# Performance work log

Hardware: AMD Instinct MI355X
Metric: run time of the kernel (lower is better)

## Reference

```python
import jax, jax.numpy as jnp
import numpy as np
from jax import lax

HIDDEN = 1024
STATE = 64
BATCH = 16
SEQ = 2048
DT_MIN, DT_MAX = 0.001, 0.1


def setup_inputs() -> dict:
    key = jax.random.key(0)
    k = jax.random.split(key, 6)
    x = jax.random.normal(k[0], (BATCH, SEQ, HIDDEN), dtype=jnp.float32)
    A = jax.random.normal(k[1], (STATE, STATE), dtype=jnp.float32) * 0.01
    B = jax.random.normal(k[2], (STATE, HIDDEN), dtype=jnp.float32) * 0.01
    C = jax.random.normal(k[3], (HIDDEN, STATE), dtype=jnp.float32) * 0.01
    D = jnp.ones((HIDDEN,), dtype=jnp.float32)
    log_dt = jax.random.uniform(k[4], (HIDDEN,), dtype=jnp.float32) * (
        np.log(DT_MAX) - np.log(DT_MIN)
    ) + np.log(DT_MIN)
    return {"x": x, "A": A, "B": B, "C": C, "D": D, "log_dt": log_dt}


def reference(x, A, B, C, D, log_dt):
    # x: (B, T, H)
    dt = jnp.exp(log_dt)                                  # (H,)
    A_bar = jax.scipy.linalg.expm(A * dt.mean())          # (N, N)
    B_bar = B * dt[None, :]                               # (N, H)
    # Precompute input injection for all timesteps: (B, T, N)
    u = jnp.einsum("bth,nh->btn", x, B_bar)

    def step(state, u_t):
        # state: (B, N); u_t: (B, N)
        state = state @ A_bar.T + u_t
        return state, state

    init = jnp.zeros((x.shape[0], A.shape[0]), dtype=x.dtype)
    _, states = lax.scan(step, init, jnp.swapaxes(u, 0, 1))  # (T, B, N)
    states = jnp.swapaxes(states, 0, 1)                      # (B, T, N)
    return jnp.einsum("btn,hn->bth", states, C) + D * x
```

## Files before the change

kernel.cpp:

```cpp
#include <hip/hip_runtime.h>


#define H   1024
#define NS  64
#define NB  16
#define TT  2048
#define LCH 64
#define KCH 32

typedef __attribute__((ext_vector_type(8))) short bf16x8;
typedef __attribute__((ext_vector_type(4))) float f32x4;
typedef __attribute__((ext_vector_type(2))) unsigned int u32x2;

#define WS_ABAR 0
#define WS_AL   4096
#define WS_F    8192
#define WS_P    40960
#define WS_U    73728
#define WS_S    2170880

__device__ __forceinline__ unsigned short f2bf(float x) {
  union { float f; unsigned u; } v; v.f = x;
  unsigned r = (v.u + 0x7FFFu + ((v.u >> 16) & 1u)) >> 16;
  return (unsigned short)r;
}

__device__ __forceinline__ bf16x8 packbf8(f32x4 a, f32x4 b) {
  bf16x8 r;
  r[0] = (short)f2bf(a[0]); r[1] = (short)f2bf(a[1]);
  r[2] = (short)f2bf(a[2]); r[3] = (short)f2bf(a[3]);
  r[4] = (short)f2bf(b[0]); r[5] = (short)f2bf(b[1]);
  r[6] = (short)f2bf(b[2]); r[7] = (short)f2bf(b[3]);
  return r;
}

__device__ __forceinline__ u32x2 packbf4(f32x4 v) {
  u32x2 r;
  r[0] = (unsigned)f2bf(v[0]) | ((unsigned)f2bf(v[1]) << 16);
  r[1] = (unsigned)f2bf(v[2]) | ((unsigned)f2bf(v[3]) << 16);
  return r;
}

__device__ __forceinline__ f32x4 mfma16(bf16x8 a, bf16x8 b, f32x4 c) {
  return __builtin_amdgcn_mfma_f32_16x16x32_bf16(a, b, c, 0, 0, 0);
}

__device__ void prep_block(const float* Ain, const float* ldt, float* ws, int which) {
  __shared__ float Mb[64 * 68];
  __shared__ short Tl[64 * 72];
  const int lane = threadIdx.x;
  const int cq = lane >> 4, cl = lane & 15;

  float s = 0.f;
  for (int j = 0; j < 16; ++j) s += expf(ldt[lane + j * 64]);
  for (int off = 32; off; off >>= 1) s += __shfl_down(s, off);
  float dtm = __shfl(s, 0) * (1.0f / 1024.0f);
  float scale = which ? dtm * (float)LCH : dtm;

  for (int idx = lane; idx < 4096; idx += 64) {
    int r = idx >> 6, c = idx & 63;
    float v = Ain[idx] * scale;
    Mb[c * 68 + r] = v;
    Tl[r * 72 + c] = (short)f2bf(v);
  }

  float E[16][4];
  for (int mt = 0; mt < 4; ++mt)
    for (int nt = 0; nt < 4; ++nt)
      for (int r = 0; r < 4; ++r) {
        int row = mt * 16 + cq * 4 + r, col = nt * 16 + cl;
        E[mt * 4 + nt][r] = (row == col ? 1.f : 0.f) + Ain[row * 64 + col] * scale;
      }

  __asm volatile("s_waitcnt lgkmcnt(0)" ::: "memory");

  for (int it = 2; it <= 12; ++it) {
    bf16x8 af[4][2];
    for (int mt = 0; mt < 4; ++mt)
      for (int kh = 0; kh < 2; ++kh)
        af[mt][kh] = *(const bf16x8*)&Tl[(mt * 16 + cl) * 72 + kh * 32 + cq * 8];
    float inv = 1.0f / (float)it;
    bf16x8 bfr[4][2];
    for (int nt = 0; nt < 4; ++nt)
      for (int kh = 0; kh < 2; ++kh) {
        const float* p = &Mb[(nt * 16 + cl) * 68 + kh * 32 + cq * 8];
        f32x4 a = *(const f32x4*)p;
        f32x4 b = *(const f32x4*)(p + 4);
        bfr[nt][kh] = packbf8(a * inv, b * inv);
      }
    f32x4 zero = {0.f, 0.f, 0.f, 0.f};
    f32x4 acc[16];
    for (int i = 0; i < 16; ++i) acc[i] = zero;
    for (int mt = 0; mt < 4; ++mt)
      for (int nt = 0; nt < 4; ++nt) {
        acc[mt * 4 + nt] = mfma16(af[mt][0], bfr[nt][0], acc[mt * 4 + nt]);
        acc[mt * 4 + nt] = mfma16(af[mt][1], bfr[nt][1], acc[mt * 4 + nt]);
      }
    __asm volatile("s_waitcnt lgkmcnt(0)" ::: "memory");
    for (int mt = 0; mt < 4; ++mt)
      for (int nt = 0; nt < 4; ++nt)
        for (int r = 0; r < 4; ++r) {
          float t = acc[mt * 4 + nt][r];
          E[mt * 4 + nt][r] += t;
          Tl[(mt * 16 + cq * 4 + r) * 72 + nt * 16 + cl] = (short)f2bf(t);
        }
    __asm volatile("s_waitcnt lgkmcnt(0)" ::: "memory");
  }

  float* dst = ws + (which ? WS_AL : WS_ABAR);
  for (int mt = 0; mt < 4; ++mt)
    for (int nt = 0; nt < 4; ++nt)
      for (int r = 0; r < 4; ++r)
        dst[(mt * 16 + cq * 4 + r) * 64 + nt * 16 + cl] = E[mt * 4 + nt][r];
}

__device__ void gemm_u(const float* x, const float* Bm, const float* ldt, float* u2, int bid) {
  __shared__ short xl[64 * 40];
  __shared__ short bl[64 * 40];
  const int tid = threadIdx.x;
  const int bt0 = bid * 64;
  const int wid = tid >> 6, lane = tid & 63;
  const int cq = lane >> 4, cl = lane & 15;
  const int mst = tid >> 2, k0 = (tid & 3) * 8;

  f32x4 zero = {0.f, 0.f, 0.f, 0.f};
  f32x4 acc[4];
  for (int i = 0; i < 4; ++i) acc[i] = zero;

  const float* xrow = x + (long)(bt0 + mst) * H + k0;
  const float* brow = Bm + (long)mst * H + k0;

  for (int hc = 0; hc < 32; ++hc) {
    int h0 = hc * 32;
    f32x4 xa = *(const f32x4*)(xrow + h0);
    f32x4 xb = *(const f32x4*)(xrow + h0 + 4);
    f32x4 ba = *(const f32x4*)(brow + h0);
    f32x4 bb = *(const f32x4*)(brow + h0 + 4);
    f32x4 da, db;
    for (int j = 0; j < 4; ++j) {
      da[j] = expf(ldt[h0 + k0 + j]);
      db[j] = expf(ldt[h0 + k0 + 4 + j]);
    }
    *(bf16x8*)&xl[mst * 40 + k0] = packbf8(xa, xb);
    *(bf16x8*)&bl[mst * 40 + k0] = packbf8(ba * da, bb * db);
    __syncthreads();
    bf16x8 afr = *(const bf16x8*)&xl[(wid * 16 + cl) * 40 + cq * 8];
    for (int nt = 0; nt < 4; ++nt) {
      bf16x8 bfr = *(const bf16x8*)&bl[(nt * 16 + cl) * 40 + cq * 8];
      acc[nt] = mfma16(afr, bfr, acc[nt]);
    }
    __syncthreads();
  }
  for (int nt = 0; nt < 4; ++nt)
    for (int r = 0; r < 4; ++r) {
      int bt = bt0 + wid * 16 + cq * 4 + r;
      int t = bt & (TT - 1), b = bt >> 11;
      u2[(long)(t * 16 + b) * 64 + nt * 16 + cl] = acc[nt][r];
    }
}

__global__ __launch_bounds__(256) void k1(const float* x, const float* Ain, const float* Bm,
                                          const float* ldt, float* ws) {
  if (blockIdx.x < 2) {
    if (threadIdx.x < 64) prep_block(Ain, ldt, ws, blockIdx.x);
    return;
  }
  gemm_u(x, Bm, ldt, ws + WS_U, blockIdx.x - 2);
}

__device__ __forceinline__ void load_RF(const float* Amat, bf16x8 Rf[4][2], int cq, int cl) {
  for (int mt = 0; mt < 4; ++mt)
    for (int kh = 0; kh < 2; ++kh) {
      int m = mt * 16 + cl;
      int kb = kh * 32 + cq * 8;
      f32x4 v0 = *(const f32x4*)&Amat[m * 64 + kb];
      f32x4 v1 = *(const f32x4*)&Amat[m * 64 + kb + 4];
      for (int j = 0; j < 4; ++j) {
        if (m == kb + j) v0[j] -= 1.f;
        if (m == kb + 4 + j) v1[j] -= 1.f;
      }
      Rf[mt][kh] = packbf8(v0, v1);
    }
}

__device__ __forceinline__ void scan_step(f32x4 Z[4], const bf16x8 Rf[4][2], short* Zl,
                                          const f32x4 U[4], int cq, int cl) {
  for (int t = 0; t < 4; ++t)
    *(u32x2*)&Zl[cl * 72 + t * 16 + cq * 4] = packbf4(Z[t]);
  __asm volatile("s_waitcnt lgkmcnt(0)" ::: "memory");
  bf16x8 zf0 = *(const bf16x8*)&Zl[cl * 72 + cq * 8];
  bf16x8 zf1 = *(const bf16x8*)&Zl[cl * 72 + 32 + cq * 8];
  for (int t = 0; t < 4; ++t) Z[t] += U[t];
  for (int mt = 0; mt < 4; ++mt) {
    Z[mt] = mfma16(Rf[mt][0], zf0, Z[mt]);
    Z[mt] = mfma16(Rf[mt][1], zf1, Z[mt]);
  }
}

__global__ __launch_bounds__(64) void scan_local_k(float* ws) {
  const float* Abar = ws + WS_ABAR;
  const float* u2 = ws + WS_U;
  float* F = ws + WS_F;
  __shared__ short Zl[16 * 72];
  const int lane = threadIdx.x, cq = lane >> 4, cl = lane & 15;
  const int c = blockIdx.x;
  bf16x8 Rf[4][2];
  load_RF(Abar, Rf, cq, cl);
  f32x4 zero = {0.f, 0.f, 0.f, 0.f};
  f32x4 Z[4], U[4], Un[4];
  for (int t = 0; t < 4; ++t) Z[t] = zero;
  const float* ub = u2 + (long)c * LCH * 1024 + cl * 64 + cq * 4;
  for (int t = 0; t < 4; ++t) U[t] = *(const f32x4*)(ub + t * 16);
  for (int ti = 0; ti < LCH; ++ti) {
    const float* un = ub + (ti + 1) * 1024;
    for (int t = 0; t < 4; ++t) Un[t] = *(const f32x4*)(un + t * 16);
    scan_step(Z, Rf, Zl, U, cq, cl);
    for (int t = 0; t < 4; ++t) U[t] = Un[t];
  }
  for (int t = 0; t < 4; ++t)
    *(f32x4*)&F[(long)c * 1024 + cl * 64 + t * 16 + cq * 4] = Z[t];
}

__global__ __launch_bounds__(64) void scan_chunks_k(float* ws) {
  const float* AL = ws + WS_AL;
  const float* F = ws + WS_F;
  float* P = ws + WS_P;
  __shared__ short Zl[16 * 72];
  const int lane = threadIdx.x, cq = lane >> 4, cl = lane & 15;
  bf16x8 Rf[4][2];
  load_RF(AL, Rf, cq, cl);
  f32x4 zero = {0.f, 0.f, 0.f, 0.f};
  f32x4 Z[4], U[4];
  for (int t = 0; t < 4; ++t) Z[t] = zero;
  for (int c = 0; c < KCH; ++c) {
    long off = (long)c * 1024 + cl * 64 + cq * 4;
    for (int t = 0; t < 4; ++t) *(f32x4*)&P[off + t * 16] = Z[t];
    for (int t = 0; t < 4; ++t) U[t] = *(const f32x4*)&F[off + t * 16];
    scan_step(Z, Rf, Zl, U, cq, cl);
  }
}

__global__ __launch_bounds__(64) void scan_final_k(float* ws) {
  const float* Abar = ws + WS_ABAR;
  const float* u2 = ws + WS_U;
  const float* P = ws + WS_P;
  float* S2 = ws + WS_S;
  __shared__ short Zl[16 * 72];
  const int lane = threadIdx.x, cq = lane >> 4, cl = lane & 15;
  const int c = blockIdx.x;
  bf16x8 Rf[4][2];
  load_RF(Abar, Rf, cq, cl);
  f32x4 Z[4], U[4], Un[4];
  long poff = (long)c * 1024 + cl * 64 + cq * 4;
  for (int t = 0; t < 4; ++t) Z[t] = *(const f32x4*)&P[poff + t * 16];
  const float* ub = u2 + (long)c * LCH * 1024 + cl * 64 + cq * 4;
  float* sb = S2 + (long)c * LCH * 1024 + cl * 64 + cq * 4;
  for (int t = 0; t < 4; ++t) U[t] = *(const f32x4*)(ub + t * 16);
  for (int ti = 0; ti < LCH; ++ti) {
    const float* un = ub + (ti + 1) * 1024;
    for (int t = 0; t < 4; ++t) Un[t] = *(const f32x4*)(un + t * 16);
    scan_step(Z, Rf, Zl, U, cq, cl);
    float* so = sb + ti * 1024;
    for (int t = 0; t < 4; ++t) *(f32x4*)(so + t * 16) = Z[t];
    for (int t = 0; t < 4; ++t) U[t] = Un[t];
  }
}

__global__ __launch_bounds__(256) void out_proj_k(const float* ws, const float* Cm,
                                                  const float* Dv, const float* x, float* out) {
  const float* S2 = ws + WS_S;
  __shared__ short sl[64 * 72];
  __shared__ short cls[128 * 72];
  const int tid = threadIdx.x;
  const int bid = blockIdx.x;
  const int bt0 = (bid & 511) * 64;
  const int h0 = (bid >> 9) * 128;
  const int wid = tid >> 6, lane = tid & 63;
  const int cq = lane >> 4, cl = lane & 15;

  {
    int m = tid >> 2, k0 = (tid & 3) * 16;
    int bt = bt0 + m, t = bt & (TT - 1), b = bt >> 11;
    const float* sr = S2 + (long)(t * 16 + b) * 64 + k0;
    f32x4 a0 = *(const f32x4*)(sr);
    f32x4 a1 = *(const f32x4*)(sr + 4);
    f32x4 a2 = *(const f32x4*)(sr + 8);
    f32x4 a3 = *(const f32x4*)(sr + 12);
    *(bf16x8*)&sl[m * 72 + k0] = packbf8(a0, a1);
    *(bf16x8*)&sl[m * 72 + k0 + 8] = packbf8(a2, a3);

    int hl = tid >> 1, kc = (tid & 1) * 32;
    const float* cr = Cm + (long)(h0 + hl) * 64 + kc;
    f32x4 c0 = *(const f32x4*)(cr);
    f32x4 c1 = *(const f32x4*)(cr + 4);
    f32x4 c2 = *(const f32x4*)(cr + 8);
    f32x4 c3 = *(const f32x4*)(cr + 12);
    f32x4 c4 = *(const f32x4*)(cr + 16);
    f32x4 c5 = *(const f32x4*)(cr + 20);
    f32x4 c6 = *(const f32x4*)(cr + 24);
    f32x4 c7 = *(const f32x4*)(cr + 28);
    *(bf16x8*)&cls[hl * 72 + kc] = packbf8(c0, c1);
    *(bf16x8*)&cls[hl * 72 + kc + 8] = packbf8(c2, c3);
    *(bf16x8*)&cls[hl * 72 + kc + 16] = packbf8(c4, c5);
    *(bf16x8*)&cls[hl * 72 + kc + 24] = packbf8(c6, c7);
  }
  __syncthreads();

  bf16x8 af0 = *(const bf16x8*)&sl[(wid * 16 + cl) * 72 + cq * 8];
  bf16x8 af1 = *(const bf16x8*)&sl[(wid * 16 + cl) * 72 + 32 + cq * 8];
  f32x4 zero = {0.f, 0.f, 0.f, 0.f};
  for (int nt = 0; nt < 8; ++nt) {
    bf16x8 b0 = *(const bf16x8*)&cls[(nt * 16 + cl) * 72 + cq * 8];
    bf16x8 b1 = *(const bf16x8*)&cls[(nt * 16 + cl) * 72 + 32 + cq * 8];
    f32x4 acc = zero;
    acc = mfma16(af0, b0, acc);
    acc = mfma16(af1, b1, acc);
    int h = h0 + nt * 16 + cl;
    float d = Dv[h];
    for (int r = 0; r < 4; ++r) {
      long bt = bt0 + wid * 16 + cq * 4 + r;
      long idx = bt * H + h;
      out[idx] = acc[r] + d * x[idx];
    }
  }
}

extern "C" void kernel_launch(void* const* d_in, const int* in_sizes, int n_in,
                              void* d_out, int out_size, void* d_ws, size_t ws_size,
                              hipStream_t stream) {
  const float* x = (const float*)d_in[0];
  const float* A = (const float*)d_in[1];
  const float* Bm = (const float*)d_in[2];
  const float* Cm = (const float*)d_in[3];
  const float* Dv = (const float*)d_in[4];
  const float* ldt = (const float*)d_in[5];
  float* out = (float*)d_out;
  float* ws = (float*)d_ws;

  k1<<<dim3(2 + 512), dim3(256), 0, stream>>>(x, A, Bm, ldt, ws);
  scan_local_k<<<dim3(KCH), dim3(64), 0, stream>>>(ws);
  scan_chunks_k<<<dim3(1), dim3(64), 0, stream>>>(ws);
  scan_final_k<<<dim3(KCH), dim3(64), 0, stream>>>(ws);
  out_proj_k<<<dim3(4096), dim3(256), 0, stream>>>(ws, Cm, Dv, x, out);
}
```

Baseline: 533.2 us.

## Pre-convert B and C to bf16, store states in bf16, drop LDS staging

A new prologue kernel computes B scaled by dt and converts B and C to bf16 once, writing them into the workspace. The u projection and the output projection now load MFMA fragments straight from global memory instead of staging through LDS with block barriers. Scan states are written as bf16 rather than fp32, which halves the state traffic between the scan and the output projection. In exchange there is one extra launch, B and C are re-read from cache by every block, and the stored states lose precision.

```diff
diff --git a/kernel.cpp b/kernel.cpp
--- a/kernel.cpp
+++ b/kernel.cpp
@@ -18,6 +18,8 @@
 #define WS_P    40960
 #define WS_U    73728
 #define WS_S    2170880
+#define WS_BBF  8192
+#define WS_CBF  3219456
 
 __device__ __forceinline__ unsigned short f2bf(float x) {
   union { float f; unsigned u; } v; v.f = x;
@@ -43,6 +45,20 @@
 
 __device__ __forceinline__ f32x4 mfma16(bf16x8 a, bf16x8 b, f32x4 c) {
   return __builtin_amdgcn_mfma_f32_16x16x32_bf16(a, b, c, 0, 0, 0);
+}
+
+__global__ __launch_bounds__(256) void k0(const float* Bm, const float* Cm,
+                                          const float* ldt, float* ws) {
+  short* Bbf = (short*)(ws + WS_BBF);
+  short* Cbf = (short*)(ws + WS_CBF);
+  const int idx = (blockIdx.x * 256 + threadIdx.x) * 4;
+  f32x4 b = *(const f32x4*)(Bm + idx);
+  f32x4 l = *(const f32x4*)(ldt + (idx & (H - 1)));
+  f32x4 bb;
+  for (int j = 0; j < 4; ++j) bb[j] = b[j] * expf(l[j]);
+  *(u32x2*)&Bbf[idx] = packbf4(bb);
+  f32x4 c = *(const f32x4*)(Cm + idx);
+  *(u32x2*)&Cbf[idx] = packbf4(c);
 }
 
 __device__ void prep_block(const float* Ain, const float* ldt, float* ws, int which) {
@@ -114,58 +130,47 @@
         dst[(mt * 16 + cq * 4 + r) * 64 + nt * 16 + cl] = E[mt * 4 + nt][r];
 }
 
-__device__ void gemm_u(const float* x, const float* Bm, const float* ldt, float* u2, int bid) {
-  __shared__ short xl[64 * 40];
-  __shared__ short bl[64 * 40];
+__device__ void gemm_u(const float* x, const float* ws, float* u2, int bid) {
+  const short* Bbf = (const short*)(ws + WS_BBF);
   const int tid = threadIdx.x;
-  const int bt0 = bid * 64;
   const int wid = tid >> 6, lane = tid & 63;
   const int cq = lane >> 4, cl = lane & 15;
-  const int mst = tid >> 2, k0 = (tid & 3) * 8;
+  const int bt0 = bid * 64 + wid * 16;
+
+  const float* xr = x + (long)(bt0 + cl) * H + cq * 8;
+  const short* br = Bbf + cq * 8;
 
   f32x4 zero = {0.f, 0.f, 0.f, 0.f};
   f32x4 acc[4];
   for (int i = 0; i < 4; ++i) acc[i] = zero;
 
-  const float* xrow = x + (long)(bt0 + mst) * H + k0;
-  const float* brow = Bm + (long)mst * H + k0;
-
-  for (int hc = 0; hc < 32; ++hc) {
-    int h0 = hc * 32;
-    f32x4 xa = *(const f32x4*)(xrow + h0);
-    f32x4 xb = *(const f32x4*)(xrow + h0 + 4);
-    f32x4 ba = *(const f32x4*)(brow + h0);
-    f32x4 bb = *(const f32x4*)(brow + h0 + 4);
-    f32x4 da, db;
-    for (int j = 0; j < 4; ++j) {
-      da[j] = expf(ldt[h0 + k0 + j]);
-      db[j] = expf(ldt[h0 + k0 + 4 + j]);
+#pragma unroll 4
+  for (int ks = 0; ks < 32; ++ks) {
+    const int k0 = ks * 32;
+    f32x4 xa = *(const f32x4*)(xr + k0);
+    f32x4 xb = *(const f32x4*)(xr + k0 + 4);
+    bf16x8 af = packbf8(xa, xb);
+    for (int nt = 0; nt < 4; ++nt) {
+      bf16x8 bf = *(const bf16x8*)(br + (nt * 16 + cl) * H + k0);
+      acc[nt] = mfma16(af, bf, acc[nt]);
     }
-    *(bf16x8*)&xl[mst * 40 + k0] = packbf8(xa, xb);
-    *(bf16x8*)&bl[mst * 40 + k0] = packbf8(ba * da, bb * db);
-    __syncthreads();
-    bf16x8 afr = *(const bf16x8*)&xl[(wid * 16 + cl) * 40 + cq * 8];
-    for (int nt = 0; nt < 4; ++nt) {
-      bf16x8 bfr = *(const bf16x8*)&bl[(nt * 16 + cl) * 40 + cq * 8];
-      acc[nt] = mfma16(afr, bfr, acc[nt]);
-    }
-    __syncthreads();
-  }
+  }
+
   for (int nt = 0; nt < 4; ++nt)
     for (int r = 0; r < 4; ++r) {
-      int bt = bt0 + wid * 16 + cq * 4 + r;
-      int t = bt & (TT - 1), b = bt >> 11;
+      int obt = bt0 + cq * 4 + r;
+      int t = obt & (TT - 1), b = obt >> 11;
       u2[(long)(t * 16 + b) * 64 + nt * 16 + cl] = acc[nt][r];
     }
 }
 
-__global__ __launch_bounds__(256) void k1(const float* x, const float* Ain, const float* Bm,
+__global__ __launch_bounds__(256) void k1(const float* x, const float* Ain,
                                           const float* ldt, float* ws) {
   if (blockIdx.x < 2) {
     if (threadIdx.x < 64) prep_block(Ain, ldt, ws, blockIdx.x);
     return;
   }
-  gemm_u(x, Bm, ldt, ws + WS_U, blockIdx.x - 2);
+  gemm_u(x, ws, ws + WS_U, blockIdx.x - 2);
 }
 
 __device__ __forceinline__ void load_RF(const float* Amat, bf16x8 Rf[4][2], int cq, int cl) {
@@ -244,7 +249,7 @@
   const float* Abar = ws + WS_ABAR;
   const float* u2 = ws + WS_U;
   const float* P = ws + WS_P;
-  float* S2 = ws + WS_S;
+  short* S2bf = (short*)(ws + WS_S);
   __shared__ short Zl[16 * 72];
   const int lane = threadIdx.x, cq = lane >> 4, cl = lane & 15;
   const int c = blockIdx.x;
@@ -254,72 +259,48 @@
   long poff = (long)c * 1024 + cl * 64 + cq * 4;
   for (int t = 0; t < 4; ++t) Z[t] = *(const f32x4*)&P[poff + t * 16];
   const float* ub = u2 + (long)c * LCH * 1024 + cl * 64 + cq * 4;
-  float* sb = S2 + (long)c * LCH * 1024 + cl * 64 + cq * 4;
+  short* sb = S2bf + (long)c * LCH * 1024 + cl * 64 + cq * 4;
   for (int t = 0; t < 4; ++t) U[t] = *(const f32x4*)(ub + t * 16);
   for (int ti = 0; ti < LCH; ++ti) {
     const float* un = ub + (ti + 1) * 1024;
     for (int t = 0; t < 4; ++t) Un[t] = *(const f32x4*)(un + t * 16);
     scan_step(Z, Rf, Zl, U, cq, cl);
-    float* so = sb + ti * 1024;
-    for (int t = 0; t < 4; ++t) *(f32x4*)(so + t * 16) = Z[t];
+    short* so = sb + ti * 1024;
+    for (int t = 0; t < 4; ++t) *(u32x2*)(so + t * 16) = packbf4(Z[t]);
     for (int t = 0; t < 4; ++t) U[t] = Un[t];
   }
 }
 
-__global__ __launch_bounds__(256) void out_proj_k(const float* ws, const float* Cm,
-                                                  const float* Dv, const float* x, float* out) {
-  const float* S2 = ws + WS_S;
-  __shared__ short sl[64 * 72];
-  __shared__ short cls[128 * 72];
+__global__ __launch_bounds__(256) void out_proj_k(const float* ws, const float* Dv,
+                                                  const float* x, float* out) {
+  const short* Sbf = (const short*)(ws + WS_S);
+  const short* Cbf = (const short*)(ws + WS_CBF);
   const int tid = threadIdx.x;
-  const int bid = blockIdx.x;
-  const int bt0 = (bid & 511) * 64;
-  const int h0 = (bid >> 9) * 128;
   const int wid = tid >> 6, lane = tid & 63;
   const int cq = lane >> 4, cl = lane & 15;
-
-  {
-    int m = tid >> 2, k0 = (tid & 3) * 16;
-    int bt = bt0 + m, t = bt & (TT - 1), b = bt >> 11;
-    const float* sr = S2 + (long)(t * 16 + b) * 64 + k0;
-    f32x4 a0 = *(const f32x4*)(sr);
-    f32x4 a1 = *(const f32x4*)(sr + 4);
-    f32x4 a2 = *(const f32x4*)(sr + 8);
-    f32x4 a3 = *(const f32x4*)(sr + 12);
-    *(bf16x8*)&sl[m * 72 + k0] = packbf8(a0, a1);
-    *(bf16x8*)&sl[m * 72 + k0 + 8] = packbf8(a2, a3);
-
-    int hl = tid >> 1, kc = (tid & 1) * 32;
-    const float* cr = Cm + (long)(h0 + hl) * 64 + kc;
-    f32x4 c0 = *(const f32x4*)(cr);
-    f32x4 c1 = *(const f32x4*)(cr + 4);
-    f32x4 c2 = *(const f32x4*)(cr + 8);
-    f32x4 c3 = *(const f32x4*)(cr + 12);
-    f32x4 c4 = *(const f32x4*)(cr + 16);
-    f32x4 c5 = *(const f32x4*)(cr + 20);
-    f32x4 c6 = *(const f32x4*)(cr + 24);
-    f32x4 c7 = *(const f32x4*)(cr + 28);
-    *(bf16x8*)&cls[hl * 72 + kc] = packbf8(c0, c1);
-    *(bf16x8*)&cls[hl * 72 + kc + 8] = packbf8(c2, c3);
-    *(bf16x8*)&cls[hl * 72 + kc + 16] = packbf8(c4, c5);
-    *(bf16x8*)&cls[hl * 72 + kc + 24] = packbf8(c6, c7);
-  }
-  __syncthreads();
-
-  bf16x8 af0 = *(const bf16x8*)&sl[(wid * 16 + cl) * 72 + cq * 8];
-  bf16x8 af1 = *(const bf16x8*)&sl[(wid * 16 + cl) * 72 + 32 + cq * 8];
-  f32x4 zero = {0.f, 0.f, 0.f, 0.f};
+  const int bid = blockIdx.x;
+  const int bt0 = (bid & 511) * 64 + wid * 16;
+  const int h0 = (bid >> 9) * 128;
+
+  const int abt = bt0 + cl;
+  const int at = abt & (TT - 1), ab = abt >> 11;
+  const short* sr = Sbf + (long)(at * 16 + ab) * 64 + cq * 8;
+  bf16x8 a0 = *(const bf16x8*)(sr);
+  bf16x8 a1 = *(const bf16x8*)(sr + 32);
+
+#pragma unroll
   for (int nt = 0; nt < 8; ++nt) {
-    bf16x8 b0 = *(const bf16x8*)&cls[(nt * 16 + cl) * 72 + cq * 8];
-    bf16x8 b1 = *(const bf16x8*)&cls[(nt * 16 + cl) * 72 + 32 + cq * 8];
-    f32x4 acc = zero;
-    acc = mfma16(af0, b0, acc);
-    acc = mfma16(af1, b1, acc);
-    int h = h0 + nt * 16 + cl;
-    float d = Dv[h];
+    const int h = h0 + nt * 16 + cl;
+    const short* cr = Cbf + (long)h * 64 + cq * 8;
+    bf16x8 b0 = *(const bf16x8*)(cr);
+    bf16x8 b1 = *(const bf16x8*)(cr + 32);
+    f32x4 acc = {0.f, 0.f, 0.f, 0.f};
+    acc = mfma16(a0, b0, acc);
+    acc = mfma16(a1, b1, acc);
+    const float d = Dv[h];
     for (int r = 0; r < 4; ++r) {
-      long bt = bt0 + wid * 16 + cq * 4 + r;
-      long idx = bt * H + h;
+      long obt = bt0 + cq * 4 + r;
+      long idx = obt * H + h;
       out[idx] = acc[r] + d * x[idx];
     }
   }
@@ -337,9 +318,10 @@
   float* out = (float*)d_out;
   float* ws = (float*)d_ws;
 
-  k1<<<dim3(2 + 512), dim3(256), 0, stream>>>(x, A, Bm, ldt, ws);
+  k0<<<dim3(64), dim3(256), 0, stream>>>(Bm, Cm, ldt, ws);
+  k1<<<dim3(2 + 512), dim3(256), 0, stream>>>(x, A, ldt, ws);
   scan_local_k<<<dim3(KCH), dim3(64), 0, stream>>>(ws);
   scan_chunks_k<<<dim3(1), dim3(64), 0, stream>>>(ws);
   scan_final_k<<<dim3(KCH), dim3(64), 0, stream>>>(ws);
-  out_proj_k<<<dim3(4096), dim3(256), 0, stream>>>(ws, Cm, Dv, x, out);
-}
+  out_proj_k<<<dim3(4096), dim3(256), 0, stream>>>(ws, Dv, x, out);
+}
```

New measurement: 507.0 us. 1.05x faster.
